# Optimization experiments

Measured on AMD Instinct MI355X. Metric: run time of the kernel, lower is better.

## Reference

```python
import jax, jax.numpy as jnp
import numpy as np


def setup_inputs() -> dict:
    key = jax.random.key(0)
    k1, k2, k3, k4, k5 = jax.random.split(key, 5)
    B, C, H, W = 16, 256, 32, 32
    G = 4
    gd = C // G
    x = jax.random.normal(k1, (B, C, H, W), dtype=jnp.float32)
    # grouped 1x1 convs == per-group [gd, gd] linear maps (torch weight (C, C//G, 1, 1))
    s = 1.0 / np.sqrt(gd)
    wq = jax.random.normal(k2, (G, gd, gd), dtype=jnp.float32) * s
    wk = jax.random.normal(k3, (G, gd, gd), dtype=jnp.float32) * s
    wv = jax.random.normal(k4, (G, gd, gd), dtype=jnp.float32) * s
    wo = jax.random.normal(k5, (C, C), dtype=jnp.float32) * (1.0 / np.sqrt(C))
    return {"x": x, "wq": wq, "wk": wk, "wv": wv, "wo": wo}


def reference(x, wq, wk, wv, wo):
    B, C, H, W = x.shape
    G, gd = wq.shape[0], wq.shape[1]
    N = H * W
    xg = x.reshape(B, G, gd, N)  # split channels into groups, flatten spatial
    # grouped 1x1 conv projections: out[d] = sum_c w[d,c] * x[c] per group
    Q = jnp.einsum('bgcn,gdc->bgdn', xg, wq)
    K = jnp.einsum('bgcn,gdc->bgdn', xg, wk)
    V = jnp.einsum('bgcn,gdc->bgdn', xg, wv)
    scale = 1.0 / (float(gd) ** 0.5)
    # scores: Q^T K over channel dim -> [B, G, N, N]
    scores = jnp.einsum('bgdn,bgdm->bgnm', Q, K) * scale
    attn = jax.nn.softmax(scores, axis=-1)
    # out[d, n] = sum_m attn[n, m] * V[d, m]  (== (attn @ V^T)^T in torch code)
    out = jnp.einsum('bgnm,bgdm->bgdn', attn, V)
    out = out.reshape(B, C, H, W)
    # out_proj: dense 1x1 conv over all channels
    return jnp.einsum('bchw,dc->bdhw', out, wo)
```

## Files before the change

### kernel.cpp

```cpp
#include <hip/hip_runtime.h>
#include <hip/hip_bf16.h>


typedef __bf16 bf16x8 __attribute__((ext_vector_type(8)));
typedef short s16x8 __attribute__((ext_vector_type(8)));
typedef short s16x4 __attribute__((ext_vector_type(4)));
typedef float f32x4 __attribute__((ext_vector_type(4)));

__device__ __forceinline__ unsigned short f2b(float f) {
  unsigned int u = __builtin_bit_cast(unsigned int, f);
  u += 0x7fffu + ((u >> 16) & 1u);
  return (unsigned short)(u >> 16);
}
__device__ __forceinline__ unsigned short bf16u(float f) {
  return __builtin_bit_cast(unsigned short, __float2bfloat16(f));
}
__device__ __forceinline__ f32x4 mfma16(s16x8 a, s16x8 b, f32x4 c) {
  return __builtin_amdgcn_mfma_f32_16x16x32_bf16(
      __builtin_bit_cast(bf16x8, a), __builtin_bit_cast(bf16x8, b), c, 0, 0, 0);
}
__device__ __forceinline__ f32x4 mfma16k16(s16x4 a, s16x4 b, f32x4 c) {
  return __builtin_amdgcn_mfma_f32_16x16x16bf16_1k(a, b, c, 0, 0, 0);
}
__device__ __forceinline__ void gload16(const void* g, void* l) {
  __builtin_amdgcn_global_load_lds((const __attribute__((address_space(1))) void*)g,
                                   (__attribute__((address_space(3))) void*)l, 16, 0, 0);
}
__device__ __forceinline__ void stage8k(const unsigned short* g, short* l, int wid, int lane) {
  gload16(g + wid * 1024 + lane * 8,       l + wid * 1024);
  gload16(g + wid * 1024 + 512 + lane * 8, l + wid * 1024 + 512);
}

__global__ __launch_bounds__(256) void cvt_prep_kernel(
    const float* __restrict__ x, const float* __restrict__ wq, const float* __restrict__ wk,
    const float* __restrict__ wv, const float* __restrict__ wo,
    unsigned short* __restrict__ XbT, unsigned short* __restrict__ Xbs,
    unsigned short* __restrict__ Mts, unsigned short* __restrict__ Ub) {
  __shared__ __align__(16) short T[64][72];
  const int f = blockIdx.x;
  const int tid = threadIdx.x;
  if (f >= 1024) {
    int pb = f - 1024;
    if (pb < 64) {
      int id = pb * 256 + tid;
      int g = id >> 12, e = (id >> 6) & 63, c = id & 63;
      const float* q = wq + g * 4096;
      const float* k = wk + g * 4096;
      float acc = 0.f;
      for (int d = 0; d < 64; ++d) acc += q[d * 64 + c] * k[d * 64 + e];
      Mts[g * 4096 + e * 64 + (c ^ ((e & 7) << 3))] = f2b(acc * 0.125f * 1.4426950408889634f);
    } else {
      int i = (pb - 64) * 256 + tid;
      int o = i >> 8, gc = i & 255, g = gc >> 6, c = gc & 63;
      const float* v = wv + g * 4096;
      const float* w = wo + o * 256 + g * 64;
      float acc = 0.f;
      for (int d = 0; d < 64; ++d) acc += w[d] * v[d * 64 + c];
      Ub[i] = f2b(acc);
    }
    return;
  }
  const int xcd = f & 7;
  const int idx = f >> 3;
  const int head = ((idx & 7) << 3) | xcd;
  const int tile = idx >> 3;
  const int chunk = head * 16 + tile;
  const float* Xg = x + (size_t)head * 65536 + tile * 64;
  for (int i = 0; i < 4; ++i) {
    int row = i * 16 + (tid >> 4);
    int col = (tid & 15) * 4;
    float4 v = *(const float4*)(Xg + (size_t)row * 1024 + col);
    ushort4 s4 = make_ushort4(f2b(v.x), f2b(v.y), f2b(v.z), f2b(v.w));
    *(ushort4*)&T[row][col] = s4;
  }
  __syncthreads();
  unsigned short* oT = XbT + (size_t)chunk * 4096;
  unsigned short* oC = Xbs + (size_t)chunk * 4096;
  for (int p = 0; p < 2; ++p) {
    int idx2 = p * 256 + tid;
    int rr = idx2 >> 3, j = idx2 & 7;
    int sb = (j ^ (rr & 7)) * 8;
    unsigned short w[8];
    for (int i = 0; i < 8; ++i) w[i] = (unsigned short)T[sb + i][rr];
    *(s16x8*)(oT + rr * 64 + j * 8) = *(s16x8*)w;
    s16x8 rv = *(const s16x8*)&T[rr][sb];
    *(s16x8*)(oC + rr * 64 + j * 8) = rv;
  }
}

__global__ __launch_bounds__(256, 2)
void attn_kernel(const unsigned short* __restrict__ XbT, const unsigned short* __restrict__ Xbs,
                 const unsigned short* __restrict__ Mts, unsigned short* __restrict__ Ast) {
  __shared__ __align__(16) short XtB[3][4096];
  __shared__ __align__(16) short XcB[3][4096];

  const int f = blockIdx.x;
  const int bg = (f & 7) + ((f >> 6) << 3);
  const int n0 = ((f >> 3) & 7) * 128;
  const int tid = threadIdx.x;
  const int wid = tid >> 6;
  const int lane = tid & 63;
  const int l15 = lane & 15, l4 = lane >> 4;
  const int swz = (l15 & 7) << 3;
  const int l4h = l4 >> 1, l4l = (l4 & 1) * 4;
  const unsigned short* xtg = XbT + (size_t)bg * 65536;
  const unsigned short* xcg = Xbs + (size_t)bg * 65536;

  stage8k(Mts + (bg & 3) * 4096, &XcB[0][0], wid, lane);
  stage8k(xtg + (size_t)(n0 >> 6) * 4096, &XtB[0][0], wid, lane);
  stage8k(xtg + (size_t)((n0 >> 6) + 1) * 4096, &XtB[1][0], wid, lane);
  __syncthreads();

  s16x8 qpB[2][2];
  {
    s16x8 bm[4][2];
    for (int eb = 0; eb < 4; ++eb)
      for (int kc = 0; kc < 2; ++kc)
        bm[eb][kc] = *(const s16x8*)&XcB[0][(eb * 16 + l15) * 64 + ((kc * 32 + l4 * 8) ^ swz)];
    for (int nt = 0; nt < 2; ++nt) {
      int q = wid * 32 + nt * 16;
      int h = q >> 6, rl = (q & 63) + l15;
      int rsw = ((rl & 7) << 3);
      s16x8 a0 = *(const s16x8*)&XtB[h][rl * 64 + ((l4 * 8) ^ rsw)];
      s16x8 a1 = *(const s16x8*)&XtB[h][rl * 64 + ((32 + l4 * 8) ^ rsw)];
      short* Qs = (q >= 64) ? &XcB[2][0] : &XtB[2][0];
      for (int eb = 0; eb < 4; ++eb) {
        f32x4 acc = {0.f, 0.f, 0.f, 0.f};
        acc = mfma16(a0, bm[eb][0], acc);
        acc = mfma16(a1, bm[eb][1], acc);
        for (int r = 0; r < 4; ++r) {
          int qrow = q + 4 * l4 + r;
          int cb2 = eb * 2 + (l15 >> 3);
          Qs[(qrow & 63) * 64 + (((cb2 ^ (qrow & 7)) << 3) | (l15 & 7))] = (short)bf16u(acc[r]);
        }
      }
    }
  }
  asm volatile("s_waitcnt lgkmcnt(0)" ::: "memory");
  __builtin_amdgcn_sched_barrier(0);
  for (int nt = 0; nt < 2; ++nt) {
    int n = wid * 32 + nt * 16 + l15;
    const short* Qs = (wid >= 2) ? &XcB[2][0] : &XtB[2][0];
    for (int kc = 0; kc < 2; ++kc)
      qpB[nt][kc] = *(const s16x8*)&Qs[(n & 63) * 64 + (((kc * 4 + l4) ^ (n & 7)) << 3)];
  }
  __syncthreads();

  stage8k(xtg,        &XtB[0][0], wid, lane);
  stage8k(xcg,        &XcB[0][0], wid, lane);
  stage8k(xtg + 4096, &XtB[1][0], wid, lane);
  stage8k(xcg + 4096, &XcB[1][0], wid, lane);

  float rowSp[2] = {0.f, 0.f};
  f32x4 acc[2][4];
  for (int nt = 0; nt < 2; ++nt)
    for (int cb = 0; cb < 4; ++cb) acc[nt][cb] = (f32x4){0.f, 0.f, 0.f, 0.f};

#define STEP(K, VMC)                                                                    \
  {                                                                                     \
    asm volatile("s_waitcnt vmcnt(" VMC ")" ::: "memory");                              \
    __builtin_amdgcn_s_barrier();                                                       \
    __builtin_amdgcn_sched_barrier(0);                                                  \
    if ((K) < 14) {                                                                     \
      stage8k(xtg + (size_t)((K) + 2) * 4096, &XtB[((K) + 2) % 3][0], wid, lane);       \
      stage8k(xcg + (size_t)((K) + 2) * 4096, &XcB[((K) + 2) % 3][0], wid, lane);       \
    }                                                                                   \
    const int cs = (K) % 3;                                                             \
    s16x8 xt0, xt1;                                                                     \
    s16x4 ax4[4][4];                                                                    \
    f32x4 s[2][4];                                                                      \
    for (int mb = 0; mb < 4; ++mb) {                                                    \
      int rm = mb * 16 + l15;                                                           \
      xt0 = *(const s16x8*)&XtB[cs][rm * 64 + ((l4 * 8) ^ swz)];                        \
      xt1 = *(const s16x8*)&XtB[cs][rm * 64 + ((32 + l4 * 8) ^ swz)];                   \
      for (int nt = 0; nt < 2; ++nt) {                                                  \
        f32x4 a = {0.f, 0.f, 0.f, 0.f};                                                 \
        a = mfma16(xt0, qpB[nt][0], a);                                                 \
        a = mfma16(xt1, qpB[nt][1], a);                                                 \
        s[nt][mb] = a;                                                                  \
      }                                                                                 \
    }                                                                                   \
    for (int cb = 0; cb < 4; ++cb) {                                                    \
      int rc = cb * 16 + l15;                                                           \
      for (int mb = 0; mb < 4; ++mb)                                                    \
        ax4[cb][mb] = *(const s16x4*)&XcB[cs][rc * 64 +                                 \
                        (((mb * 2 + l4h) ^ (rc & 7)) << 3) + l4l];                      \
    }                                                                                   \
    for (int nt = 0; nt < 2; ++nt) {                                                    \
      float ps = 0.f;                                                                   \
      for (int mb = 0; mb < 4; ++mb) {                                                  \
        float p0 = __builtin_amdgcn_exp2f(s[nt][mb][0]);                                \
        float p1 = __builtin_amdgcn_exp2f(s[nt][mb][1]);                                \
        float p2 = __builtin_amdgcn_exp2f(s[nt][mb][2]);                                \
        float p3 = __builtin_amdgcn_exp2f(s[nt][mb][3]);                                \
        ps += (p0 + p1) + (p2 + p3);                                                    \
        unsigned int lo = (unsigned int)bf16u(p0) | ((unsigned int)bf16u(p1) << 16);    \
        unsigned int hi = (unsigned int)bf16u(p2) | ((unsigned int)bf16u(p3) << 16);    \
        uint2 pu; pu.x = lo; pu.y = hi;                                                 \
        s16x4 pb = __builtin_bit_cast(s16x4, pu);                                       \
        for (int cb = 0; cb < 4; ++cb)                                                  \
          acc[nt][cb] = mfma16k16(ax4[cb][mb], pb, acc[nt][cb]);                        \
      }                                                                                 \
      rowSp[nt] += ps;                                                                  \
    }                                                                                   \
  }

  STEP(0, "4")  STEP(1, "4")  STEP(2, "4")  STEP(3, "4")
  STEP(4, "4")  STEP(5, "4")  STEP(6, "4")  STEP(7, "4")
  STEP(8, "4")  STEP(9, "4")  STEP(10, "4") STEP(11, "4")
  STEP(12, "4") STEP(13, "4") STEP(14, "4") STEP(15, "0")
#undef STEP

  const int b = bg >> 2, g = bg & 3;
  for (int nt = 0; nt < 2; ++nt) {
    float t = rowSp[nt];
    t += __shfl_xor(t, 16, 64);
    t += __shfl_xor(t, 32, 64);
    float inv = 1.f / t;
    int n = n0 + wid * 32 + nt * 16 + l15;
    unsigned short* Ag = Ast + ((size_t)(b * 1024 + n)) * 256 + g * 64;
    for (int cb = 0; cb < 4; ++cb) {
      f32x4 v = acc[nt][cb];
      ushort4 pk = make_ushort4(bf16u(v[0] * inv), bf16u(v[1] * inv),
                                bf16u(v[2] * inv), bf16u(v[3] * inv));
      *(ushort4*)(Ag + cb * 16 + l4 * 4) = pk;
    }
  }
}

__global__ __launch_bounds__(256, 2)
void proj_kernel(const unsigned short* __restrict__ Ub, const unsigned short* __restrict__ Ast,
                 float* __restrict__ out) {
  const int b = blockIdx.z;
  const int o0 = blockIdx.y * 128;
  const int n0 = blockIdx.x * 128;
  const int tid = threadIdx.x;
  const int wid = tid >> 6;
  const int lane = tid & 63;
  const int l15 = lane & 15, l4 = lane >> 4;
  const int ow = o0 + (wid & 1) * 64;
  const int nw = n0 + (wid >> 1) * 64;
  const unsigned short* A_ = Ast + ((size_t)b * 1024 + nw) * 256;

  f32x4 acc[4][4];
  for (int i = 0; i < 4; ++i)
    for (int j = 0; j < 4; ++j) acc[i][j] = (f32x4){0.f, 0.f, 0.f, 0.f};

  for (int kc = 0; kc < 8; ++kc) {
    s16x8 af[4], bfr[4];
    for (int ob = 0; ob < 4; ++ob)
      af[ob] = *(const s16x8*)(Ub + (size_t)(ow + ob * 16 + l15) * 256 + kc * 32 + l4 * 8);
    for (int nb = 0; nb < 4; ++nb)
      bfr[nb] = *(const s16x8*)(A_ + (size_t)(nb * 16 + l15) * 256 + kc * 32 + l4 * 8);
    for (int ob = 0; ob < 4; ++ob)
      for (int nb = 0; nb < 4; ++nb)
        acc[ob][nb] = mfma16(af[ob], bfr[nb], acc[ob][nb]);
  }
  float* O = out + ((size_t)b * 256 + ow) * 1024 + nw;
  for (int ob = 0; ob < 4; ++ob)
    for (int r = 0; r < 4; ++r)
      for (int nb = 0; nb < 4; ++nb)
        O[(size_t)(ob * 16 + l4 * 4 + r) * 1024 + nb * 16 + l15] = acc[ob][nb][r];
}

extern "C" void kernel_launch(void* const* d_in, const int* in_sizes, int n_in,
                              void* d_out, int out_size, void* d_ws, size_t ws_size,
                              hipStream_t stream) {
  const float* x  = (const float*)d_in[0];
  const float* wq = (const float*)d_in[1];
  const float* wk = (const float*)d_in[2];
  const float* wv = (const float*)d_in[3];
  const float* wo = (const float*)d_in[4];
  float* out = (float*)d_out;
  char* ws = (char*)d_ws;
  unsigned short* XbT = (unsigned short*)(ws);
  unsigned short* Xbs = (unsigned short*)(ws + 8388608);
  unsigned short* Mts = (unsigned short*)(ws + 16777216);
  unsigned short* Ub  = (unsigned short*)(ws + 16777216 + 32768);
  unsigned short* Ast = (unsigned short*)(ws + 16777216 + 163840);

  cvt_prep_kernel<<<1344, 256, 0, stream>>>(x, wq, wk, wv, wo, XbT, Xbs, Mts, Ub);
  attn_kernel<<<512, 256, 0, stream>>>(XbT, Xbs, Mts, Ast);
  proj_kernel<<<dim3(8, 2, 16), 256, 0, stream>>>(Ub, Ast, out);
}
```

Before: 53.15 us.

## Split attention key dimension across waves with LDS cross-wave reduction

Each wave now covers all 128 query rows for a 16-key slice of every tile, where before it owned 32 query rows across all keys. This cuts per-wave LDS reads of the key and value tiles, and each wave holds 8 query fragments in registers. A cross-wave reduction through LDS then sums partial outputs and row sums before normalization. In exchange, accumulator registers grow fourfold (128 floats per lane), which risks spills or lower occupancy, and the epilogue gains extra barriers and scratch traffic.

```diff
diff --git a/kernel.cpp b/kernel.cpp
--- a/kernel.cpp
+++ b/kernel.cpp
@@ -91,8 +91,7 @@
 __global__ __launch_bounds__(256, 2)
 void attn_kernel(const unsigned short* __restrict__ XbT, const unsigned short* __restrict__ Xbs,
                  const unsigned short* __restrict__ Mts, unsigned short* __restrict__ Ast) {
-  __shared__ __align__(16) short XtB[3][4096];
-  __shared__ __align__(16) short XcB[3][4096];
+  __shared__ __align__(16) short XB[6][4096];
 
   const int f = blockIdx.x;
   const int bg = (f & 7) + ((f >> 6) << 3);
@@ -103,57 +102,65 @@
   const int l15 = lane & 15, l4 = lane >> 4;
   const int swz = (l15 & 7) << 3;
   const int l4h = l4 >> 1, l4l = (l4 & 1) * 4;
+  const int rm = wid * 16 + l15;
   const unsigned short* xtg = XbT + (size_t)bg * 65536;
   const unsigned short* xcg = Xbs + (size_t)bg * 65536;
 
-  stage8k(Mts + (bg & 3) * 4096, &XcB[0][0], wid, lane);
-  stage8k(xtg + (size_t)(n0 >> 6) * 4096, &XtB[0][0], wid, lane);
-  stage8k(xtg + (size_t)((n0 >> 6) + 1) * 4096, &XtB[1][0], wid, lane);
-  __syncthreads();
-
-  s16x8 qpB[2][2];
+  stage8k(Mts + (bg & 3) * 4096, &XB[3][0], wid, lane);
+  stage8k(xtg + (size_t)(n0 >> 6) * 4096, &XB[0][0], wid, lane);
+  stage8k(xtg + (size_t)((n0 >> 6) + 1) * 4096, &XB[1][0], wid, lane);
+  __syncthreads();
+
+  s16x8 qpB[8][2];
   {
     s16x8 bm[4][2];
     for (int eb = 0; eb < 4; ++eb)
       for (int kc = 0; kc < 2; ++kc)
-        bm[eb][kc] = *(const s16x8*)&XcB[0][(eb * 16 + l15) * 64 + ((kc * 32 + l4 * 8) ^ swz)];
+        bm[eb][kc] = *(const s16x8*)&XB[3][(eb * 16 + l15) * 64 + ((kc * 32 + l4 * 8) ^ swz)];
     for (int nt = 0; nt < 2; ++nt) {
       int q = wid * 32 + nt * 16;
       int h = q >> 6, rl = (q & 63) + l15;
       int rsw = ((rl & 7) << 3);
-      s16x8 a0 = *(const s16x8*)&XtB[h][rl * 64 + ((l4 * 8) ^ rsw)];
-      s16x8 a1 = *(const s16x8*)&XtB[h][rl * 64 + ((32 + l4 * 8) ^ rsw)];
-      short* Qs = (q >= 64) ? &XcB[2][0] : &XtB[2][0];
+      s16x8 a0 = *(const s16x8*)&XB[h][rl * 64 + ((l4 * 8) ^ rsw)];
+      s16x8 a1 = *(const s16x8*)&XB[h][rl * 64 + ((32 + l4 * 8) ^ rsw)];
+      short* Qs = (q >= 64) ? &XB[5][0] : &XB[2][0];
       for (int eb = 0; eb < 4; ++eb) {
-        f32x4 acc = {0.f, 0.f, 0.f, 0.f};
-        acc = mfma16(a0, bm[eb][0], acc);
-        acc = mfma16(a1, bm[eb][1], acc);
+        f32x4 acc0 = {0.f, 0.f, 0.f, 0.f};
+        acc0 = mfma16(a0, bm[eb][0], acc0);
+        acc0 = mfma16(a1, bm[eb][1], acc0);
         for (int r = 0; r < 4; ++r) {
           int qrow = q + 4 * l4 + r;
           int cb2 = eb * 2 + (l15 >> 3);
-          Qs[(qrow & 63) * 64 + (((cb2 ^ (qrow & 7)) << 3) | (l15 & 7))] = (short)bf16u(acc[r]);
+          Qs[(qrow & 63) * 64 + (((cb2 ^ (qrow & 7)) << 3) | (l15 & 7))] = (short)bf16u(acc0[r]);
         }
       }
     }
   }
   asm volatile("s_waitcnt lgkmcnt(0)" ::: "memory");
   __builtin_amdgcn_sched_barrier(0);
-  for (int nt = 0; nt < 2; ++nt) {
-    int n = wid * 32 + nt * 16 + l15;
-    const short* Qs = (wid >= 2) ? &XcB[2][0] : &XtB[2][0];
+  __syncthreads();
+#pragma unroll
+  for (int nt = 0; nt < 8; ++nt) {
+    const short* Qs = (nt < 4) ? &XB[2][0] : &XB[5][0];
+    int row = (nt & 3) * 16 + l15;
+#pragma unroll
     for (int kc = 0; kc < 2; ++kc)
-      qpB[nt][kc] = *(const s16x8*)&Qs[(n & 63) * 64 + (((kc * 4 + l4) ^ (n & 7)) << 3)];
-  }
-  __syncthreads();
-
-  stage8k(xtg,        &XtB[0][0], wid, lane);
-  stage8k(xcg,        &XcB[0][0], wid, lane);
-  stage8k(xtg + 4096, &XtB[1][0], wid, lane);
-  stage8k(xcg + 4096, &XcB[1][0], wid, lane);
-
-  float rowSp[2] = {0.f, 0.f};
-  f32x4 acc[2][4];
-  for (int nt = 0; nt < 2; ++nt)
+      qpB[nt][kc] = *(const s16x8*)&Qs[row * 64 + (((kc * 4 + l4) ^ (l15 & 7)) << 3)];
+  }
+  __syncthreads();
+
+  stage8k(xtg,        &XB[0][0], wid, lane);
+  stage8k(xcg,        &XB[3][0], wid, lane);
+  stage8k(xtg + 4096, &XB[1][0], wid, lane);
+  stage8k(xcg + 4096, &XB[4][0], wid, lane);
+
+  float rowSp[8];
+#pragma unroll
+  for (int nt = 0; nt < 8; ++nt) rowSp[nt] = 0.f;
+  f32x4 acc[8][4];
+#pragma unroll
+  for (int nt = 0; nt < 8; ++nt)
+#pragma unroll
     for (int cb = 0; cb < 4; ++cb) acc[nt][cb] = (f32x4){0.f, 0.f, 0.f, 0.f};
 
 #define STEP(K, VMC)                                                                    \
@@ -162,46 +169,36 @@
     __builtin_amdgcn_s_barrier();                                                       \
     __builtin_amdgcn_sched_barrier(0);                                                  \
     if ((K) < 14) {                                                                     \
-      stage8k(xtg + (size_t)((K) + 2) * 4096, &XtB[((K) + 2) % 3][0], wid, lane);       \
-      stage8k(xcg + (size_t)((K) + 2) * 4096, &XcB[((K) + 2) % 3][0], wid, lane);       \
+      stage8k(xtg + (size_t)((K) + 2) * 4096, &XB[((K) + 2) % 3][0], wid, lane);        \
+      stage8k(xcg + (size_t)((K) + 2) * 4096, &XB[3 + ((K) + 2) % 3][0], wid, lane);    \
     }                                                                                   \
     const int cs = (K) % 3;                                                             \
-    s16x8 xt0, xt1;                                                                     \
-    s16x4 ax4[4][4];                                                                    \
-    f32x4 s[2][4];                                                                      \
-    for (int mb = 0; mb < 4; ++mb) {                                                    \
-      int rm = mb * 16 + l15;                                                           \
-      xt0 = *(const s16x8*)&XtB[cs][rm * 64 + ((l4 * 8) ^ swz)];                        \
-      xt1 = *(const s16x8*)&XtB[cs][rm * 64 + ((32 + l4 * 8) ^ swz)];                   \
-      for (int nt = 0; nt < 2; ++nt) {                                                  \
-        f32x4 a = {0.f, 0.f, 0.f, 0.f};                                                 \
-        a = mfma16(xt0, qpB[nt][0], a);                                                 \
-        a = mfma16(xt1, qpB[nt][1], a);                                                 \
-        s[nt][mb] = a;                                                                  \
-      }                                                                                 \
-    }                                                                                   \
+    s16x8 xt0 = *(const s16x8*)&XB[cs][rm * 64 + ((l4 * 8) ^ swz)];                     \
+    s16x8 xt1 = *(const s16x8*)&XB[cs][rm * 64 + ((32 + l4 * 8) ^ swz)];                \
+    s16x4 ax4[4];                                                                       \
+    _Pragma("unroll")                                                                   \
     for (int cb = 0; cb < 4; ++cb) {                                                    \
       int rc = cb * 16 + l15;                                                           \
-      for (int mb = 0; mb < 4; ++mb)                                                    \
-        ax4[cb][mb] = *(const s16x4*)&XcB[cs][rc * 64 +                                 \
-                        (((mb * 2 + l4h) ^ (rc & 7)) << 3) + l4l];                      \
+      ax4[cb] = *(const s16x4*)&XB[3 + cs][rc * 64 +                                    \
+                    (((wid * 2 + l4h) ^ (rc & 7)) << 3) + l4l];                         \
     }                                                                                   \
-    for (int nt = 0; nt < 2; ++nt) {                                                    \
-      float ps = 0.f;                                                                   \
-      for (int mb = 0; mb < 4; ++mb) {                                                  \
-        float p0 = __builtin_amdgcn_exp2f(s[nt][mb][0]);                                \
-        float p1 = __builtin_amdgcn_exp2f(s[nt][mb][1]);                                \
-        float p2 = __builtin_amdgcn_exp2f(s[nt][mb][2]);                                \
-        float p3 = __builtin_amdgcn_exp2f(s[nt][mb][3]);                                \
-        ps += (p0 + p1) + (p2 + p3);                                                    \
-        unsigned int lo = (unsigned int)bf16u(p0) | ((unsigned int)bf16u(p1) << 16);    \
-        unsigned int hi = (unsigned int)bf16u(p2) | ((unsigned int)bf16u(p3) << 16);    \
-        uint2 pu; pu.x = lo; pu.y = hi;                                                 \
-        s16x4 pb = __builtin_bit_cast(s16x4, pu);                                       \
-        for (int cb = 0; cb < 4; ++cb)                                                  \
-          acc[nt][cb] = mfma16k16(ax4[cb][mb], pb, acc[nt][cb]);                        \
-      }                                                                                 \
-      rowSp[nt] += ps;                                                                  \
+    _Pragma("unroll")                                                                   \
+    for (int nt = 0; nt < 8; ++nt) {                                                    \
+      f32x4 sv = {0.f, 0.f, 0.f, 0.f};                                                  \
+      sv = mfma16(xt0, qpB[nt][0], sv);                                                 \
+      sv = mfma16(xt1, qpB[nt][1], sv);                                                 \
+      float p0 = __builtin_amdgcn_exp2f(sv[0]);                                         \
+      float p1 = __builtin_amdgcn_exp2f(sv[1]);                                         \
+      float p2 = __builtin_amdgcn_exp2f(sv[2]);                                         \
+      float p3 = __builtin_amdgcn_exp2f(sv[3]);                                         \
+      rowSp[nt] += (p0 + p1) + (p2 + p3);                                               \
+      unsigned int lo = (unsigned int)bf16u(p0) | ((unsigned int)bf16u(p1) << 16);      \
+      unsigned int hi = (unsigned int)bf16u(p2) | ((unsigned int)bf16u(p3) << 16);      \
+      uint2 pu; pu.x = lo; pu.y = hi;                                                   \
+      s16x4 pb = __builtin_bit_cast(s16x4, pu);                                         \
+      _Pragma("unroll")                                                                 \
+      for (int cb = 0; cb < 4; ++cb)                                                    \
+        acc[nt][cb] = mfma16k16(ax4[cb], pb, acc[nt][cb]);                              \
     }                                                                                   \
   }
 
@@ -211,19 +208,62 @@
   STEP(12, "4") STEP(13, "4") STEP(14, "4") STEP(15, "0")
 #undef STEP
 
-  const int b = bg >> 2, g = bg & 3;
-  for (int nt = 0; nt < 2; ++nt) {
+  __syncthreads();
+  float* Scr = (float*)&XB[0][0];
+
+#pragma unroll
+  for (int nt = 0; nt < 8; ++nt) {
     float t = rowSp[nt];
     t += __shfl_xor(t, 16, 64);
     t += __shfl_xor(t, 32, 64);
-    float inv = 1.f / t;
-    int n = n0 + wid * 32 + nt * 16 + l15;
-    unsigned short* Ag = Ast + ((size_t)(b * 1024 + n)) * 256 + g * 64;
-    for (int cb = 0; cb < 4; ++cb) {
-      f32x4 v = acc[nt][cb];
-      ushort4 pk = make_ushort4(bf16u(v[0] * inv), bf16u(v[1] * inv),
-                                bf16u(v[2] * inv), bf16u(v[3] * inv));
-      *(ushort4*)(Ag + cb * 16 + l4 * 4) = pk;
+    Scr[wid * 128 + nt * 16 + l15] = t;
+  }
+  __syncthreads();
+  float inv[8];
+#pragma unroll
+  for (int nt = 0; nt < 8; ++nt)
+    inv[nt] = 1.f / (Scr[nt * 16 + l15] + Scr[128 + nt * 16 + l15] +
+                     Scr[256 + nt * 16 + l15] + Scr[384 + nt * 16 + l15]);
+
+  const int b = bg >> 2, g = bg & 3;
+#pragma unroll
+  for (int rnd = 0; rnd < 2; ++rnd) {
+    __syncthreads();
+#pragma unroll
+    for (int ntl = 0; ntl < 4; ++ntl) {
+      int nt = rnd * 4 + ntl;
+#pragma unroll
+      for (int cb = 0; cb < 4; ++cb) {
+        if (cb == wid) continue;
+        int slot = wid - (wid > cb ? 1 : 0);
+        int base = ((ntl * 4 + cb) * 3 + slot) * 256;
+#pragma unroll
+        for (int r = 0; r < 4; ++r) {
+          int c = l4 * 4 + r;
+          Scr[base + c * 16 + ((l15 + c) & 15)] = acc[nt][cb][r];
+        }
+      }
+    }
+    __syncthreads();
+#pragma unroll
+    for (int ntl = 0; ntl < 4; ++ntl) {
+      int nt = rnd * 4 + ntl;
+      float v0 = acc[nt][wid][0], v1 = acc[nt][wid][1];
+      float v2 = acc[nt][wid][2], v3 = acc[nt][wid][3];
+#pragma unroll
+      for (int slot = 0; slot < 3; ++slot) {
+        int base = ((ntl * 4 + wid) * 3 + slot) * 256;
+        int c0 = l4 * 4;
+        v0 += Scr[base + c0 * 16 + ((l15 + c0) & 15)];
+        v1 += Scr[base + (c0 + 1) * 16 + ((l15 + c0 + 1) & 15)];
+        v2 += Scr[base + (c0 + 2) * 16 + ((l15 + c0 + 2) & 15)];
+        v3 += Scr[base + (c0 + 3) * 16 + ((l15 + c0 + 3) & 15)];
+      }
+      int n = n0 + nt * 16 + l15;
+      unsigned short* Ag = Ast + ((size_t)(b * 1024 + n)) * 256 + g * 64 + wid * 16 + l4 * 4;
+      ushort4 pk = make_ushort4(bf16u(v0 * inv[nt]), bf16u(v1 * inv[nt]),
+                                bf16u(v2 * inv[nt]), bf16u(v3 * inv[nt]));
+      *(ushort4*)Ag = pk;
     }
   }
 }
```

Result: slower. 93.06 us (+75.1%).
